# Performance work log

Hardware: AMD Instinct MI355X
Metric: run time of the kernel (lower is better)

The kernel has to match this reference:

```python
import jax, jax.numpy as jnp
import numpy as np

B, T, D = 256, 500, 3   # batch, time steps, input features (time, mag, err)
U, C = 512, 10          # PhasedLSTM units, n_classes
R_ON = 0.05             # open ratio of the phased time gate
ALPHA = 1e-3            # leak rate during closed phase
LN_EPS = 1e-3           # keras LayerNormalization default epsilon


def _glorot(key, shape):
    lim = np.sqrt(6.0 / (shape[0] + shape[1])).astype(np.float32)
    return jax.random.uniform(key, shape, jnp.float32, -lim, lim)


def setup_inputs() -> dict:
    key = jax.random.key(0)
    ks = jax.random.split(key, 12)
    x = jax.random.normal(ks[0], (B, T, D), jnp.float32)
    # monotonically increasing observation times per sample
    times = jnp.cumsum(jax.random.uniform(ks[1], (B, T), jnp.float32), axis=1)
    # layer 0 PhasedLSTM params (gate order i, f, g, o)
    W0 = _glorot(ks[2], (D, 4 * U)); R0 = _glorot(ks[3], (U, 4 * U)); b0 = jnp.zeros((4 * U,), jnp.float32)
    tau0 = jnp.exp(jax.random.uniform(ks[4], (U,), jnp.float32, 0.0, 3.0))
    s0 = jax.random.uniform(ks[5], (U,), jnp.float32) * tau0
    # layer 1
    W1 = _glorot(ks[6], (U, 4 * U)); R1 = _glorot(ks[7], (U, 4 * U)); b1 = jnp.zeros((4 * U,), jnp.float32)
    tau1 = jnp.exp(jax.random.uniform(ks[8], (U,), jnp.float32, 0.0, 3.0))
    s1 = jax.random.uniform(ks[9], (U,), jnp.float32) * tau1
    # per-layer LayerNorm params
    g0 = jnp.ones((U,), jnp.float32); be0 = jnp.zeros((U,), jnp.float32)
    g1 = jnp.ones((U,), jnp.float32); be1 = jnp.zeros((U,), jnp.float32)
    # classifier head
    Wf = _glorot(ks[10], (U, C)); bf = jnp.zeros((C,), jnp.float32)
    return dict(x=x, times=times, W0=W0, R0=R0, b0=b0, tau0=tau0, s0=s0, g0=g0, be0=be0,
                W1=W1, R1=R1, b1=b1, tau1=tau1, s1=s1, g1=g1, be1=be1, Wf=Wf, bf=bf)


def _layernorm(h, g, b):
    m = jnp.mean(h, axis=-1, keepdims=True)
    v = jnp.var(h, axis=-1, keepdims=True)
    return (h - m) * jax.lax.rsqrt(v + LN_EPS) * g + b


def _time_gate(t, tau, s):
    # t: [B], tau/s: [U] -> k: [B, U]
    phi = jnp.mod(t[:, None] - s, tau) / tau
    return jnp.where(phi < 0.5 * R_ON, 2.0 * phi / R_ON,
                     jnp.where(phi < R_ON, 2.0 - 2.0 * phi / R_ON, ALPHA * phi))


def _plstm_step(xi, ti, h, c, W, R, b, tau, s):
    z = xi @ W + h @ R + b                       # [B, 4U]
    i, f, g, o = jnp.split(z, 4, axis=-1)
    i = jax.nn.sigmoid(i); f = jax.nn.sigmoid(f); o = jax.nn.sigmoid(o)
    c_new = f * c + i * jnp.tanh(g)
    h_new = o * jnp.tanh(c_new)
    k = _time_gate(ti, tau, s)                   # phased time gate
    return k * h_new + (1.0 - k) * h, k * c_new + (1.0 - k) * c


def reference(x, times, W0, R0, b0, tau0, s0, g0, be0,
              W1, R1, b1, tau1, s1, g1, be1, Wf, bf):
    xt = jnp.transpose(x, (1, 0, 2))  # [T, B, D]
    tt = times.T                      # [T, B]
    zeros = jnp.zeros((x.shape[0], U), x.dtype)
    init = (zeros, zeros, zeros, zeros)

    def step(carry, inp):
        h0, c0, h1, c1 = carry
        xi, ti = inp
        h0n, c0n = _plstm_step(xi, ti, h0, c0, W0, R0, b0, tau0, s0)
        a0 = _layernorm(h0n, g0, be0)   # normed output feeds next layer; raw state is carried
        h1n, c1n = _plstm_step(a0, ti, h1, c1, W1, R1, b1, tau1, s1)
        a1 = _layernorm(h1n, g1, be1)
        probs = jax.nn.softmax(a1 @ Wf + bf)  # dropout is identity at inference
        return (h0n, c0n, h1n, c1n), probs

    _, out = jax.lax.scan(step, init, (xt, tt))  # out: [T, B, C]
    return jnp.transpose(out, (1, 0, 2))
```

## Files before the change

kernel.cpp:

```cpp
#include <hip/hip_runtime.h>
#include <hip/hip_bf16.h>


#define NB 256
#define NTHR 384
#define T_STEPS 500
#define RON 0.05f
#define ALPHA_LEAK 1e-3f

typedef short short8 __attribute__((ext_vector_type(8)));
typedef float f32x4 __attribute__((ext_vector_type(4)));
typedef unsigned long long ull;

#define OFF_WSWZ 0u
#define OFF_U1   6291456u
#define OFF_V1   6299648u
#define OFF_WFP  6307840u
#define OFF_UFV  6328320u
#define OFF_H0B  6328448u
#define OFF_H1B  6852736u
#define OFF_ST0  7377024u
#define OFF_ST1  7508096u
#define OFF_FLG0 7639168u
#define OFF_FLG1 7640192u
#define ZERO_BYTES 1312768u

#define SMEM_BYTES 156160

#define AT_LD(p)    __hip_atomic_load((p), __ATOMIC_RELAXED, __HIP_MEMORY_SCOPE_AGENT)
#define AT_ST(p, v) __hip_atomic_store((p), (v), __ATOMIC_RELAXED, __HIP_MEMORY_SCOPE_AGENT)

#define G2L(gp, lp) \
  __builtin_amdgcn_global_load_lds( \
      (const __attribute__((address_space(1))) void*)(gp), \
      (__attribute__((address_space(3))) void*)(lp), 16, 0, 16)

__device__ __forceinline__ short f2bf(float x) {
  unsigned u = __float_as_uint(x);
  unsigned r = (u + 0x7fffu + ((u >> 16) & 1u)) >> 16;
  return (short)r;
}
__device__ __forceinline__ float bf2f(short s) {
  return __uint_as_float(((unsigned)(unsigned short)s) << 16);
}
__device__ __forceinline__ float sigm(float x) { return 1.f / (1.f + __expf(-x)); }
__device__ __forceinline__ float tanh_f(float x) {
  float cx = fminf(fmaxf(x, -15.f), 15.f);
  float e = __expf(2.f * cx);
  return (e - 1.f) / (e + 1.f);
}
__device__ __forceinline__ float timegate(float t, float tau, float s) {
  float phi = fmodf(t - s, tau);
  if (phi < 0.f) phi += tau;
  phi /= tau;
  return phi < 0.5f * RON ? (2.f / RON) * phi
       : (phi < RON ? 2.f - (2.f / RON) * phi : ALPHA_LEAK * phi);
}
__device__ __forceinline__ int fragidx(int m, int k) {
  return ((((k >> 5) * 2 + (m >> 4)) * 64) + (((k >> 3) & 3) * 16) + (m & 15)) * 8 + (k & 7);
}

__global__ void prep_weights(const float* __restrict__ R0, const float* __restrict__ W1,
                             const float* __restrict__ R1, const float* __restrict__ g0,
                             short* __restrict__ Wswz) {
  int t = blockIdx.x * 256 + threadIdx.x;
  int lane = t & 63; int rest = t >> 6;
  int nf = rest & 1;  rest >>= 1;
  int kb = rest & 15; rest >>= 4;
  int ch = rest & 1;  rest >>= 1;
  int mm = rest % 3;  int slice = rest / 3;
  int c = ch * 32 + nf * 16 + (lane & 15);
  int gate = c >> 4;
  int unit = slice * 16 + (c & 15);
  int gcol = gate * 512 + unit;
  int k0 = kb * 32 + (lane >> 4) * 8;
  const float* src = (mm == 0) ? R0 : (mm == 1 ? W1 : R1);
  short8 o;
  #pragma unroll
  for (int e = 0; e < 8; ++e) {
    float v = src[(size_t)(k0 + e) * 2048 + gcol];
    if (mm == 1) v *= g0[k0 + e];
    o[e] = f2bf(v);
  }
  *(short8*)(Wswz + (size_t)t * 8) = o;
}

__global__ void prep_vecs(const float* __restrict__ W1, const float* __restrict__ g0,
                          const float* __restrict__ be0,
                          float* __restrict__ u1, float* __restrict__ v1) {
  int c = blockIdx.x * 256 + threadIdx.x;
  float su = 0.f, sv = 0.f;
  for (int k = 0; k < 512; ++k) {
    float w = W1[(size_t)k * 2048 + c];
    su += be0[k] * w; sv += g0[k] * w;
  }
  u1[c] = su; v1[c] = sv;
}

__global__ void prep_head(const float* __restrict__ Wf, const float* __restrict__ g1,
                          const float* __restrict__ be1, const float* __restrict__ bfv,
                          float* __restrict__ Wfp, float* __restrict__ ufv) {
  int t = blockIdx.x * 256 + threadIdx.x;
  if (t < 5120) {
    int kk = t / 640, rem = t - kk * 640, c = rem >> 6, l = rem & 63;
    int k = 8 * l + kk;
    Wfp[t] = g1[k] * Wf[k * 10 + c];
  }
  if (t < 10) {
    float su = bfv[t], sv = 0.f;
    for (int k = 0; k < 512; ++k) {
      float w = Wf[k * 10 + t];
      su += be1[k] * w; sv += g1[k] * w;
    }
    ufv[t] = su; ufv[16 + t] = sv;
  }
}

struct Ptrs {
  const float *x, *times, *W0, *b0, *tau0, *s0, *b1, *tau1, *s1;
  const float *u1v, *v1v, *Wfp, *ufv;
  short *H0b, *H1b;
  float *St0, *St1;
  unsigned *flag0, *flag1;
  float *out;
};

__launch_bounds__(NTHR, 1)
__global__ void plstm_persist(Ptrs P, const short* __restrict__ Wswz) {
  extern __shared__ char smem[];
  short* h0b  = (short*)smem;
  short* h1bL = (short*)(smem + 32768);
  float* h0f  = (float*)(smem + 98304);
  float* c0f = h0f + 512;
  float* h1f = h0f + 1024;
  float* c1f = h0f + 1536;
  float* mu0 = (float*)(smem + 106496); float* rs0 = mu0 + 32;
  float* mu1 = mu0 + 64;                float* rs1 = mu0 + 96;
  float* zbv = (float*)(smem + 107008);
  float* prm = (float*)(smem + 132736);
  float* wfl = (float*)(smem + 134784);
  float* ufl = (float*)(smem + 155264);
  float* xtb = (float*)(smem + 155392);
  float* xtb1 = (float*)(smem + 155904);

  const int tid = threadIdx.x;
  const int g = blockIdx.x & 7;
  const int slice = blockIdx.x >> 3;
  const int wid = tid >> 6, lane = tid & 63;
  const int mm = wid >> 1, ch = wid & 1;
  const int gm0 = g * 32;

  for (int i = tid; i < 2048; i += NTHR) h0f[i] = 0.f;
  for (int i = tid; i < 512; i += NTHR) {
    float v;
    if (i < 192)      { int f = i >> 6, c = i & 63; v = P.W0[f * 2048 + ((c >> 4) << 9) + slice * 16 + (c & 15)]; }
    else if (i < 256) { int c = i & 63; v = P.b0[((c >> 4) << 9) + slice * 16 + (c & 15)]; }
    else if (i < 320) { int c = i & 63; int gc = ((c >> 4) << 9) + slice * 16 + (c & 15);
                        v = P.b1[gc] + P.u1v[gc]; }
    else if (i < 384) { int c = i & 63; v = P.v1v[((c >> 4) << 9) + slice * 16 + (c & 15)]; }
    else if (i < 448) v = 0.f;
    else if (i < 464) v = P.tau0[slice * 16 + (i & 15)];
    else if (i < 480) v = P.s0[slice * 16 + (i & 15)];
    else if (i < 496) v = P.tau1[slice * 16 + (i & 15)];
    else              v = P.s1[slice * 16 + (i & 15)];
    prm[i] = v;
  }
  for (int i = tid; i < 5120; i += NTHR) wfl[i] = P.Wfp[i];
  if (tid < 32) ufl[tid] = P.ufv[tid];

  short8 wr[16][2];
  {
    const short* wb = Wswz + ((((size_t)slice * 3 + mm) * 2 + ch) * 32 * 64) * 8;
    #pragma unroll
    for (int kb = 0; kb < 16; ++kb)
      #pragma unroll
      for (int nf = 0; nf < 2; ++nf) {
        wr[kb][nf] = *(const short8*)(wb + ((kb * 2 + nf) * 64 + lane) * 8);
        asm volatile("" : "+v"(wr[kb][nf]));
      }
  }
  __syncthreads();

  for (int r = 0; r < T_STEPS + 2; ++r) {
    const int bufA = (r + 1) & 1;
    const int bufB = r & 1;
    short* h1s = h1bL + bufB * 16384;

    if (wid == 0) {
      const unsigned tgt = (unsigned)r;
      const unsigned* fp = P.flag0 + g * 32 + (lane & 31);
      for (int it_ = 0; it_ < 100000; ++it_) {
        unsigned v = (lane < 32) ? AT_LD(fp) : 0xFFFFFFFFu;
        if (__all((int)(v >= tgt))) break;
        __builtin_amdgcn_s_sleep(1);
      }
    } else if (wid == 4) {
      int m = lane & 31;
      if (lane < 32) {
        int step = (r < T_STEPS) ? r : (T_STEPS - 1);
        const float* xp = P.x + ((size_t)(gm0 + m) * T_STEPS + step) * 3;
        xtb[m * 4 + 0] = xp[0];
        xtb[m * 4 + 1] = xp[1];
        xtb[m * 4 + 2] = xp[2];
        xtb[m * 4 + 3] = P.times[(size_t)(gm0 + m) * T_STEPS + step];
      } else {
        int s1_ = (r >= 1) ? (r - 1) : 0;
        xtb1[m] = P.times[(size_t)(gm0 + m) * T_STEPS + s1_];
      }
    }
    __syncthreads();

    if (tid < 256) {
      const char* gA = (const char*)(P.H0b + ((size_t)bufA * 8 + g) * 16384);
      const char* gB = (const char*)(P.H1b + ((size_t)bufB * 8 + g) * 16384);
      char* lA = (char*)h0b;
      char* lB = (char*)h1s;
      #pragma unroll
      for (int k = 0; k < 8; ++k) {
        size_t off = (size_t)(k * 256 + tid) * 16;
        G2L(gA + off, lA + off);
        G2L(gB + off, lB + off);
      }
    } else if (wid == 5) {
      const int layer = lane >> 5, m = lane & 31;
      const float* base = layer ? (P.St1 + ((size_t)bufB * 8 + g) * 2048 + m * 64)
                                : (P.St0 + ((size_t)bufA * 8 + g) * 2048 + m * 64);
      const ull* bu = (const ull*)base;
      float s_ = 0.f, q_ = 0.f;
      #pragma unroll
      for (int sl = 0; sl < 32; ++sl) {
        ull v = AT_LD(bu + sl);
        s_ += __uint_as_float((unsigned)v);
        q_ += __uint_as_float((unsigned)(v >> 32));
      }
      float mu = s_ * (1.f / 512.f);
      float var = q_ * (1.f / 512.f) - mu * mu;
      float rs = rsqrtf(var + 1e-3f);
      if (layer == 0) { mu0[m] = mu; rs0[m] = rs; }
      else            { mu1[m] = mu; rs1[m] = rs; }
    }
    __syncthreads();
    float m1r = 0.f, r1r = 0.f;
    if (wid == 1) { m1r = mu1[slice]; r1r = rs1[slice]; }

    {
      f32x4 acc[2][2] = {};
      const short* asrc = (mm == 2) ? h1s : h0b;
      #pragma unroll
      for (int kb = 0; kb < 16; ++kb) {
        short8 a0 = *(const short8*)(asrc + ((kb * 2 + 0) * 64 + lane) * 8);
        short8 a1 = *(const short8*)(asrc + ((kb * 2 + 1) * 64 + lane) * 8);
        #pragma unroll
        for (int nf = 0; nf < 2; ++nf) {
          acc[0][nf] = __builtin_amdgcn_mfma_f32_16x16x32_bf16(a0, wr[kb][nf], acc[0][nf], 0, 0, 0);
          acc[1][nf] = __builtin_amdgcn_mfma_f32_16x16x32_bf16(a1, wr[kb][nf], acc[1][nf], 0, 0, 0);
        }
      }
      float* z = zbv + mm * 2144;
      #pragma unroll
      for (int mf = 0; mf < 2; ++mf)
        #pragma unroll
        for (int nf = 0; nf < 2; ++nf)
          #pragma unroll
          for (int q = 0; q < 4; ++q) {
            int row = mf * 16 + (lane >> 4) * 4 + q;
            int col = ch * 32 + nf * 16 + (lane & 15);
            z[row * 67 + col] = acc[mf][nf][q];
          }
    }
    __syncthreads();

    const bool l0act = (r < T_STEPS);
    const bool l1act = (r >= 1 && r <= T_STEPS);
    if (tid < 256 && l0act) {
      int m = tid >> 3, u0 = (tid & 7) << 1;
      float x0 = xtb[m * 4 + 0], x1 = xtb[m * 4 + 1], x2 = xtb[m * 4 + 2];
      float tmv = xtb[m * 4 + 3];
      unsigned pack = 0;
      float hnv[2];
      #pragma unroll
      for (int uu = 0; uu < 2; ++uu) {
        int u = u0 + uu, id = m * 16 + u;
        float zg4[4];
        #pragma unroll
        for (int q = 0; q < 4; ++q) {
          int c = q * 16 + u;
          zg4[q] = zbv[m * 67 + c] + prm[192 + c]
                 + x0 * prm[c] + x1 * prm[64 + c] + x2 * prm[128 + c];
        }
        float iv = sigm(zg4[0]), fv = sigm(zg4[1]), gv = tanh_f(zg4[2]), ov = sigm(zg4[3]);
        float cold = c0f[id], hold = h0f[id];
        float cp = fv * cold + iv * gv;
        float hp = ov * tanh_f(cp);
        float k = timegate(tmv, prm[448 + u], prm[464 + u]);
        float hn = k * hp + (1.f - k) * hold;
        float cn = k * cp + (1.f - k) * cold;
        h0f[id] = hn; c0f[id] = cn; hnv[uu] = hn;
        pack |= ((unsigned)(unsigned short)f2bf(hn)) << (16 * uu);
      }
      AT_ST((unsigned*)(P.H0b + ((size_t)bufB * 8 + g) * 16384 + fragidx(m, slice * 16 + u0)), pack);
      float sr = hnv[0] + hnv[1], qr = hnv[0] * hnv[0] + hnv[1] * hnv[1];
      sr += __shfl_down(sr, 4, 8); qr += __shfl_down(qr, 4, 8);
      sr += __shfl_down(sr, 2, 8); qr += __shfl_down(qr, 2, 8);
      sr += __shfl_down(sr, 1, 8); qr += __shfl_down(qr, 1, 8);
      if ((tid & 7) == 0) {
        ull pv = ((ull)__float_as_uint(qr) << 32) | __float_as_uint(sr);
        AT_ST((ull*)(P.St0 + ((size_t)bufB * 8 + g) * 2048) + m * 32 + slice, pv);
      }
    }
    #pragma unroll
    for (int pass = 0; pass < 2; ++pass) {
      int idx = -1;
      if (pass == 0 && tid >= 256) idx = tid - 256;
      if (pass == 1 && tid < 128)  idx = 128 + tid;
      if (idx >= 0 && l1act) {
        int m = idx >> 3, u0 = (idx & 7) << 1;
        float mu0m = mu0[m], rs0m = rs0[m];
        float tmv = xtb1[m];
        unsigned pack = 0;
        float hnv[2];
        #pragma unroll
        for (int uu = 0; uu < 2; ++uu) {
          int u = u0 + uu, id = m * 16 + u;
          float zg4[4];
          #pragma unroll
          for (int q = 0; q < 4; ++q) {
            int c = q * 16 + u;
            float zA = zbv[2144 + m * 67 + c];
            float zB = zbv[4288 + m * 67 + c];
            zg4[q] = rs0m * zA + zB + prm[256 + c] - mu0m * rs0m * prm[320 + c];
          }
          float iv = sigm(zg4[0]), fv = sigm(zg4[1]), gv = tanh_f(zg4[2]), ov = sigm(zg4[3]);
          float cold = c1f[id], hold = h1f[id];
          float cp = fv * cold + iv * gv;
          float hp = ov * tanh_f(cp);
          float k = timegate(tmv, prm[480 + u], prm[496 + u]);
          float hn = k * hp + (1.f - k) * hold;
          float cn = k * cp + (1.f - k) * cold;
          h1f[id] = hn; c1f[id] = cn; hnv[uu] = hn;
          pack |= ((unsigned)(unsigned short)f2bf(hn)) << (16 * uu);
        }
        AT_ST((unsigned*)(P.H1b + ((size_t)bufA * 8 + g) * 16384 + fragidx(m, slice * 16 + u0)), pack);
        float sr = hnv[0] + hnv[1], qr = hnv[0] * hnv[0] + hnv[1] * hnv[1];
        sr += __shfl_down(sr, 4, 8); qr += __shfl_down(qr, 4, 8);
        sr += __shfl_down(sr, 2, 8); qr += __shfl_down(qr, 2, 8);
        sr += __shfl_down(sr, 1, 8); qr += __shfl_down(qr, 1, 8);
        if ((idx & 7) == 0) {
          ull pv = ((ull)__float_as_uint(qr) << 32) | __float_as_uint(sr);
          AT_ST((ull*)(P.St1 + ((size_t)bufA * 8 + g) * 2048) + m * 32 + slice, pv);
        }
      }
    }
    __syncthreads();

    if (tid == 0 && r <= T_STEPS) {
      AT_ST(P.flag0 + g * 32 + slice, (unsigned)(r + 1));
    }
    if (wid == 1 && r >= 2) {
      int msam = slice;
      short8 hv8 = *(const short8*)(h1s + fragidx(msam, lane * 8));
      float lg[10];
      #pragma unroll
      for (int c = 0; c < 10; ++c) lg[c] = 0.f;
      #pragma unroll
      for (int kk = 0; kk < 8; ++kk) {
        float hv = bf2f(hv8[kk]);
        const float* wf = wfl + kk * 640 + lane;
        #pragma unroll
        for (int c = 0; c < 10; ++c) lg[c] += hv * wf[c * 64];
      }
      #pragma unroll
      for (int off = 32; off > 0; off >>= 1)
        #pragma unroll
        for (int c = 0; c < 10; ++c) lg[c] += __shfl_down(lg[c], off, 64);
      if (lane == 0) {
        float logit[10], mx = -1e30f;
        #pragma unroll
        for (int c = 0; c < 10; ++c) {
          logit[c] = r1r * lg[c] + ufl[c] - m1r * r1r * ufl[16 + c];
          mx = fmaxf(mx, logit[c]);
        }
        float ssum = 0.f;
        #pragma unroll
        for (int c = 0; c < 10; ++c) { logit[c] = expf(logit[c] - mx); ssum += logit[c]; }
        float inv = 1.f / ssum;
        float* op = P.out + ((size_t)(gm0 + msam) * T_STEPS + (r - 2)) * 10;
        #pragma unroll
        for (int c = 0; c < 10; ++c) op[c] = logit[c] * inv;
      }
    }
  }
}

extern "C" void kernel_launch(void* const* d_in, const int* in_sizes, int n_in,
                              void* d_out, int out_size, void* d_ws, size_t ws_size,
                              hipStream_t stream) {
  const float* x    = (const float*)d_in[0];
  const float* tms  = (const float*)d_in[1];
  const float* W0   = (const float*)d_in[2];
  const float* R0   = (const float*)d_in[3];
  const float* b0   = (const float*)d_in[4];
  const float* tau0 = (const float*)d_in[5];
  const float* s0   = (const float*)d_in[6];
  const float* g0   = (const float*)d_in[7];
  const float* be0  = (const float*)d_in[8];
  const float* W1   = (const float*)d_in[9];
  const float* R1   = (const float*)d_in[10];
  const float* b1   = (const float*)d_in[11];
  const float* tau1 = (const float*)d_in[12];
  const float* s1   = (const float*)d_in[13];
  const float* g1   = (const float*)d_in[14];
  const float* be1  = (const float*)d_in[15];
  const float* Wf   = (const float*)d_in[16];
  const float* bfv  = (const float*)d_in[17];

  char* ws = (char*)d_ws;
  short* Wswz = (short*)(ws + OFF_WSWZ);
  float* u1m  = (float*)(ws + OFF_U1);
  float* v1m  = (float*)(ws + OFF_V1);
  float* Wfpm = (float*)(ws + OFF_WFP);
  float* ufvm = (float*)(ws + OFF_UFV);

  Ptrs P;
  P.x = x; P.times = tms; P.W0 = W0; P.b0 = b0; P.tau0 = tau0; P.s0 = s0;
  P.b1 = b1; P.tau1 = tau1; P.s1 = s1;
  P.u1v = u1m; P.v1v = v1m; P.Wfp = Wfpm; P.ufv = ufvm;
  P.H0b = (short*)(ws + OFF_H0B);
  P.H1b = (short*)(ws + OFF_H1B);
  P.St0 = (float*)(ws + OFF_ST0);
  P.St1 = (float*)(ws + OFF_ST1);
  P.flag0 = (unsigned*)(ws + OFF_FLG0);
  P.flag1 = (unsigned*)(ws + OFF_FLG1);
  P.out = (float*)d_out;

  hipFuncSetAttribute(reinterpret_cast<const void*>(plstm_persist),
                      hipFuncAttributeMaxDynamicSharedMemorySize, SMEM_BYTES);

  prep_weights<<<1536, 256, 0, stream>>>(R0, W1, R1, g0, Wswz);
  prep_vecs<<<8, 256, 0, stream>>>(W1, g0, be0, u1m, v1m);
  prep_head<<<20, 256, 0, stream>>>(Wf, g1, be1, bfv, Wfpm, ufvm);
  hipMemsetAsync(ws + OFF_H0B, 0, ZERO_BYTES, stream);
  plstm_persist<<<NB, NTHR, SMEM_BYTES, stream>>>(P, Wswz);
}
```

Before: 5.245 ms.

## Split each block into two 16-sample half-groups and overlap sync/loads with MFMA

Each persistent block now handles two independent 16-sample sub-groups and alternates between them. While six warps run the recurrent MFMAs and gate math for one sub-group, two extra warps wait on that sub-group's flags, prefetch its hidden state into LDS, and compute LayerNorm statistics for the other. The goal is to hide the cross-block flag wait and global-to-LDS latency behind compute instead of serialising them every step. In exchange the block uses more threads, more double-buffered LDS, and a more involved per-half phase schedule, and each MFMA now uses only a single 16-row fragment.

```diff
diff --git a/kernel.cpp b/kernel.cpp
--- a/kernel.cpp
+++ b/kernel.cpp
@@ -3,7 +3,7 @@
 
 
 #define NB 256
-#define NTHR 384
+#define NTHR 512
 #define T_STEPS 500
 #define RON 0.05f
 #define ALPHA_LEAK 1e-3f
@@ -21,11 +21,10 @@
 #define OFF_H1B  6852736u
 #define OFF_ST0  7377024u
 #define OFF_ST1  7508096u
-#define OFF_FLG0 7639168u
-#define OFF_FLG1 7640192u
+#define OFF_FLG  7639168u
 #define ZERO_BYTES 1312768u
 
-#define SMEM_BYTES 156160
+#define SMEM_BYTES 143872
 
 #define AT_LD(p)    __hip_atomic_load((p), __ATOMIC_RELAXED, __HIP_MEMORY_SCOPE_AGENT)
 #define AT_ST(p, v) __hip_atomic_store((p), (v), __ATOMIC_RELAXED, __HIP_MEMORY_SCOPE_AGENT)
@@ -56,8 +55,8 @@
   return phi < 0.5f * RON ? (2.f / RON) * phi
        : (phi < RON ? 2.f - (2.f / RON) * phi : ALPHA_LEAK * phi);
 }
-__device__ __forceinline__ int fragidx(int m, int k) {
-  return ((((k >> 5) * 2 + (m >> 4)) * 64) + (((k >> 3) & 3) * 16) + (m & 15)) * 8 + (k & 7);
+__device__ __forceinline__ int fragidx16(int m, int k) {
+  return ((k >> 5) * 64 + ((k >> 3) & 3) * 16 + m) * 8 + (k & 7);
 }
 
 __global__ void prep_weights(const float* __restrict__ R0, const float* __restrict__ W1,
@@ -121,36 +120,32 @@
   const float *u1v, *v1v, *Wfp, *ufv;
   short *H0b, *H1b;
   float *St0, *St1;
-  unsigned *flag0, *flag1;
+  unsigned *flag;
   float *out;
 };
 
 __launch_bounds__(NTHR, 1)
 __global__ void plstm_persist(Ptrs P, const short* __restrict__ Wswz) {
   extern __shared__ char smem[];
-  short* h0b  = (short*)smem;
-  short* h1bL = (short*)(smem + 32768);
-  float* h0f  = (float*)(smem + 98304);
-  float* c0f = h0f + 512;
-  float* h1f = h0f + 1024;
-  float* c1f = h0f + 1536;
-  float* mu0 = (float*)(smem + 106496); float* rs0 = mu0 + 32;
-  float* mu1 = mu0 + 64;                float* rs1 = mu0 + 96;
-  float* zbv = (float*)(smem + 107008);
-  float* prm = (float*)(smem + 132736);
-  float* wfl = (float*)(smem + 134784);
-  float* ufl = (float*)(smem + 155264);
-  float* xtb = (float*)(smem + 155392);
-  float* xtb1 = (float*)(smem + 155904);
+  short* h0bs[2] = {(short*)smem, (short*)(smem + 16384)};
+  short* h1bs[2] = {(short*)(smem + 32768), (short*)(smem + 65536)};
+  float* zbv    = (float*)(smem + 98304);
+  float* sts[2] = {(float*)(smem + 111360), (float*)(smem + 115456)};
+  float* mus[2] = {(float*)(smem + 119552), (float*)(smem + 119808)};
+  float* prm    = (float*)(smem + 120064);
+  float* wfl    = (float*)(smem + 122112);
+  float* ufl    = (float*)(smem + 142592);
+  float* xts[2] = {(float*)(smem + 142720), (float*)(smem + 143232)};
 
   const int tid = threadIdx.x;
-  const int g = blockIdx.x & 7;
+  const int pair = blockIdx.x & 7;
   const int slice = blockIdx.x >> 3;
   const int wid = tid >> 6, lane = tid & 63;
   const int mm = wid >> 1, ch = wid & 1;
-  const int gm0 = g * 32;
-
-  for (int i = tid; i < 2048; i += NTHR) h0f[i] = 0.f;
+  const int qgrp[2] = {pair * 2, pair * 2 + 1};
+
+  for (int i = tid; i < 1024; i += NTHR) { sts[0][i] = 0.f; }
+  for (int i = tid; i < 1024; i += NTHR) { sts[1][i] = 0.f; }
   for (int i = tid; i < 512; i += NTHR) {
     float v;
     if (i < 192)      { int f = i >> 6, c = i & 63; v = P.W0[f * 2048 + ((c >> 4) << 9) + slice * 16 + (c & 15)]; }
@@ -169,7 +164,7 @@
   if (tid < 32) ufl[tid] = P.ufv[tid];
 
   short8 wr[16][2];
-  {
+  if (wid < 6) {
     const short* wb = Wswz + ((((size_t)slice * 3 + mm) * 2 + ch) * 32 * 64) * 8;
     #pragma unroll
     for (int kb = 0; kb < 16; ++kb)
@@ -181,212 +176,208 @@
   }
   __syncthreads();
 
-  for (int r = 0; r < T_STEPS + 2; ++r) {
-    const int bufA = (r + 1) & 1;
-    const int bufB = r & 1;
-    short* h1s = h1bL + bufB * 16384;
-
-    if (wid == 0) {
-      const unsigned tgt = (unsigned)r;
-      const unsigned* fp = P.flag0 + g * 32 + (lane & 31);
-      for (int it_ = 0; it_ < 100000; ++it_) {
-        unsigned v = (lane < 32) ? AT_LD(fp) : 0xFFFFFFFFu;
-        if (__all((int)(v >= tgt))) break;
-        __builtin_amdgcn_s_sleep(1);
-      }
-    } else if (wid == 4) {
-      int m = lane & 31;
-      if (lane < 32) {
-        int step = (r < T_STEPS) ? r : (T_STEPS - 1);
-        const float* xp = P.x + ((size_t)(gm0 + m) * T_STEPS + step) * 3;
-        xtb[m * 4 + 0] = xp[0];
-        xtb[m * 4 + 1] = xp[1];
-        xtb[m * 4 + 2] = xp[2];
-        xtb[m * 4 + 3] = P.times[(size_t)(gm0 + m) * T_STEPS + step];
-      } else {
-        int s1_ = (r >= 1) ? (r - 1) : 0;
-        xtb1[m] = P.times[(size_t)(gm0 + m) * T_STEPS + s1_];
-      }
-    }
-    __syncthreads();
-
-    if (tid < 256) {
-      const char* gA = (const char*)(P.H0b + ((size_t)bufA * 8 + g) * 16384);
-      const char* gB = (const char*)(P.H1b + ((size_t)bufB * 8 + g) * 16384);
-      char* lA = (char*)h0b;
-      char* lB = (char*)h1s;
-      #pragma unroll
-      for (int k = 0; k < 8; ++k) {
-        size_t off = (size_t)(k * 256 + tid) * 16;
-        G2L(gA + off, lA + off);
-        G2L(gB + off, lB + off);
-      }
-    } else if (wid == 5) {
-      const int layer = lane >> 5, m = lane & 31;
-      const float* base = layer ? (P.St1 + ((size_t)bufB * 8 + g) * 2048 + m * 64)
-                                : (P.St0 + ((size_t)bufA * 8 + g) * 2048 + m * 64);
-      const ull* bu = (const ull*)base;
-      float s_ = 0.f, q_ = 0.f;
-      #pragma unroll
-      for (int sl = 0; sl < 32; ++sl) {
-        ull v = AT_LD(bu + sl);
-        s_ += __uint_as_float((unsigned)v);
-        q_ += __uint_as_float((unsigned)(v >> 32));
-      }
-      float mu = s_ * (1.f / 512.f);
-      float var = q_ * (1.f / 512.f) - mu * mu;
-      float rs = rsqrtf(var + 1e-3f);
-      if (layer == 0) { mu0[m] = mu; rs0[m] = rs; }
-      else            { mu1[m] = mu; rs1[m] = rs; }
-    }
-    __syncthreads();
-    float m1r = 0.f, r1r = 0.f;
-    if (wid == 1) { m1r = mu1[slice]; r1r = rs1[slice]; }
-
-    {
-      f32x4 acc[2][2] = {};
-      const short* asrc = (mm == 2) ? h1s : h0b;
-      #pragma unroll
-      for (int kb = 0; kb < 16; ++kb) {
-        short8 a0 = *(const short8*)(asrc + ((kb * 2 + 0) * 64 + lane) * 8);
-        short8 a1 = *(const short8*)(asrc + ((kb * 2 + 1) * 64 + lane) * 8);
-        #pragma unroll
-        for (int nf = 0; nf < 2; ++nf) {
-          acc[0][nf] = __builtin_amdgcn_mfma_f32_16x16x32_bf16(a0, wr[kb][nf], acc[0][nf], 0, 0, 0);
-          acc[1][nf] = __builtin_amdgcn_mfma_f32_16x16x32_bf16(a1, wr[kb][nf], acc[1][nf], 0, 0, 0);
+  for (int i = 0; i <= T_STEPS + 2; ++i) {
+    #pragma unroll
+    for (int h = 0; h < 2; ++h) {
+      const int X = h, Y = h ^ 1;
+      const int rs_ = i;
+      const int rc_ = (h == 0) ? i - 1 : i;
+      const bool sv  = (rs_ <= T_STEPS + 1);
+      const bool cv  = (rc_ >= 0 && rc_ <= T_STEPS + 1);
+      const bool mfv = (rc_ >= 0 && rc_ <= T_STEPS);
+      const int qX = qgrp[X], qY = qgrp[Y];
+
+      if (wid < 6) {
+        if (mfv) {
+          f32x4 acc[2] = {};
+          const short* asrc = (mm == 2) ? (h1bs[Y] + (rc_ & 1) * 8192) : h0bs[Y];
+          #pragma unroll
+          for (int kb = 0; kb < 16; ++kb) {
+            short8 a = *(const short8*)(asrc + (kb * 64 + lane) * 8);
+            acc[0] = __builtin_amdgcn_mfma_f32_16x16x32_bf16(a, wr[kb][0], acc[0], 0, 0, 0);
+            acc[1] = __builtin_amdgcn_mfma_f32_16x16x32_bf16(a, wr[kb][1], acc[1], 0, 0, 0);
+          }
+          float* z = zbv + mm * 1088;
+          #pragma unroll
+          for (int nf = 0; nf < 2; ++nf)
+            #pragma unroll
+            for (int q = 0; q < 4; ++q)
+              z[((lane >> 4) * 4 + q) * 67 + ch * 32 + nf * 16 + (lane & 15)] = acc[nf][q];
+        }
+      } else if (sv) {
+        {
+          const unsigned tgt = (unsigned)rs_;
+          const unsigned* fp = P.flag + qX * 32 + (lane & 31);
+          for (int it_ = 0; it_ < 100000; ++it_) {
+            unsigned v = (lane < 32) ? AT_LD(fp) : 0xFFFFFFFFu;
+            if (__all((int)(v >= tgt))) break;
+            __builtin_amdgcn_s_sleep(1);
+          }
+        }
+        const int bufAs = (rs_ + 1) & 1, bufBs = rs_ & 1;
+        if (wid == 6) {
+          const char* gA = (const char*)(P.H0b + ((size_t)bufAs * 16 + qX) * 8192);
+          const char* gB = (const char*)(P.H1b + ((size_t)bufBs * 16 + qX) * 8192);
+          char* lA = (char*)h0bs[X];
+          char* lB = (char*)(h1bs[X] + (rs_ & 1) * 8192);
+          #pragma unroll
+          for (int j = 0; j < 16; ++j) {
+            unsigned off = j * 1024u + (unsigned)lane * 16u;
+            G2L(gA + off, lA + off);
+            G2L(gB + off, lB + off);
+          }
+          int m = lane & 15;
+          if (lane < 16) {
+            int step = (rs_ < T_STEPS) ? rs_ : (T_STEPS - 1);
+            const float* xp = P.x + ((size_t)(qX * 16 + m) * T_STEPS + step) * 3;
+            float* xt = xts[X];
+            xt[m * 4 + 0] = xp[0]; xt[m * 4 + 1] = xp[1]; xt[m * 4 + 2] = xp[2];
+            xt[m * 4 + 3] = P.times[(size_t)(qX * 16 + m) * T_STEPS + step];
+          } else if (lane < 32) {
+            int s1_ = (rs_ >= 1) ? rs_ - 1 : 0;
+            if (s1_ > T_STEPS - 1) s1_ = T_STEPS - 1;
+            xts[X][64 + m] = P.times[(size_t)(qX * 16 + m) * T_STEPS + s1_];
+          }
+        } else {
+          const int layer = lane >> 5, m = lane & 31;
+          if (m < 16) {
+            const float* base = layer
+                ? (P.St1 + ((size_t)bufBs * 16 + qX) * 1024 + m * 64)
+                : (P.St0 + ((size_t)bufAs * 16 + qX) * 1024 + m * 64);
+            const ull* bu = (const ull*)base;
+            float s_ = 0.f, q_ = 0.f;
+            #pragma unroll
+            for (int sl = 0; sl < 32; ++sl) {
+              ull v = AT_LD(bu + sl);
+              s_ += __uint_as_float((unsigned)v);
+              q_ += __uint_as_float((unsigned)(v >> 32));
+            }
+            float mu = s_ * (1.f / 512.f);
+            float var = q_ * (1.f / 512.f) - mu * mu;
+            mus[X][layer * 32 + m] = mu;
+            mus[X][layer * 32 + 16 + m] = rsqrtf(var + 1e-3f);
+          }
         }
       }
-      float* z = zbv + mm * 2144;
-      #pragma unroll
-      for (int mf = 0; mf < 2; ++mf)
-        #pragma unroll
-        for (int nf = 0; nf < 2; ++nf)
-          #pragma unroll
-          for (int q = 0; q < 4; ++q) {
-            int row = mf * 16 + (lane >> 4) * 4 + q;
-            int col = ch * 32 + nf * 16 + (lane & 15);
-            z[row * 67 + col] = acc[mf][nf][q];
-          }
-    }
-    __syncthreads();
-
-    const bool l0act = (r < T_STEPS);
-    const bool l1act = (r >= 1 && r <= T_STEPS);
-    if (tid < 256 && l0act) {
-      int m = tid >> 3, u0 = (tid & 7) << 1;
-      float x0 = xtb[m * 4 + 0], x1 = xtb[m * 4 + 1], x2 = xtb[m * 4 + 2];
-      float tmv = xtb[m * 4 + 3];
-      unsigned pack = 0;
-      float hnv[2];
-      #pragma unroll
-      for (int uu = 0; uu < 2; ++uu) {
-        int u = u0 + uu, id = m * 16 + u;
-        float zg4[4];
-        #pragma unroll
-        for (int q = 0; q < 4; ++q) {
-          int c = q * 16 + u;
-          zg4[q] = zbv[m * 67 + c] + prm[192 + c]
-                 + x0 * prm[c] + x1 * prm[64 + c] + x2 * prm[128 + c];
-        }
-        float iv = sigm(zg4[0]), fv = sigm(zg4[1]), gv = tanh_f(zg4[2]), ov = sigm(zg4[3]);
-        float cold = c0f[id], hold = h0f[id];
-        float cp = fv * cold + iv * gv;
-        float hp = ov * tanh_f(cp);
-        float k = timegate(tmv, prm[448 + u], prm[464 + u]);
-        float hn = k * hp + (1.f - k) * hold;
-        float cn = k * cp + (1.f - k) * cold;
-        h0f[id] = hn; c0f[id] = cn; hnv[uu] = hn;
-        pack |= ((unsigned)(unsigned short)f2bf(hn)) << (16 * uu);
-      }
-      AT_ST((unsigned*)(P.H0b + ((size_t)bufB * 8 + g) * 16384 + fragidx(m, slice * 16 + u0)), pack);
-      float sr = hnv[0] + hnv[1], qr = hnv[0] * hnv[0] + hnv[1] * hnv[1];
-      sr += __shfl_down(sr, 4, 8); qr += __shfl_down(qr, 4, 8);
-      sr += __shfl_down(sr, 2, 8); qr += __shfl_down(qr, 2, 8);
-      sr += __shfl_down(sr, 1, 8); qr += __shfl_down(qr, 1, 8);
-      if ((tid & 7) == 0) {
-        ull pv = ((ull)__float_as_uint(qr) << 32) | __float_as_uint(sr);
-        AT_ST((ull*)(P.St0 + ((size_t)bufB * 8 + g) * 2048) + m * 32 + slice, pv);
-      }
-    }
-    #pragma unroll
-    for (int pass = 0; pass < 2; ++pass) {
-      int idx = -1;
-      if (pass == 0 && tid >= 256) idx = tid - 256;
-      if (pass == 1 && tid < 128)  idx = 128 + tid;
-      if (idx >= 0 && l1act) {
-        int m = idx >> 3, u0 = (idx & 7) << 1;
-        float mu0m = mu0[m], rs0m = rs0[m];
-        float tmv = xtb1[m];
-        unsigned pack = 0;
-        float hnv[2];
-        #pragma unroll
-        for (int uu = 0; uu < 2; ++uu) {
-          int u = u0 + uu, id = m * 16 + u;
-          float zg4[4];
-          #pragma unroll
-          for (int q = 0; q < 4; ++q) {
-            int c = q * 16 + u;
-            float zA = zbv[2144 + m * 67 + c];
-            float zB = zbv[4288 + m * 67 + c];
-            zg4[q] = rs0m * zA + zB + prm[256 + c] - mu0m * rs0m * prm[320 + c];
-          }
-          float iv = sigm(zg4[0]), fv = sigm(zg4[1]), gv = tanh_f(zg4[2]), ov = sigm(zg4[3]);
-          float cold = c1f[id], hold = h1f[id];
-          float cp = fv * cold + iv * gv;
-          float hp = ov * tanh_f(cp);
-          float k = timegate(tmv, prm[480 + u], prm[496 + u]);
-          float hn = k * hp + (1.f - k) * hold;
-          float cn = k * cp + (1.f - k) * cold;
-          h1f[id] = hn; c1f[id] = cn; hnv[uu] = hn;
-          pack |= ((unsigned)(unsigned short)f2bf(hn)) << (16 * uu);
-        }
-        AT_ST((unsigned*)(P.H1b + ((size_t)bufA * 8 + g) * 16384 + fragidx(m, slice * 16 + u0)), pack);
-        float sr = hnv[0] + hnv[1], qr = hnv[0] * hnv[0] + hnv[1] * hnv[1];
-        sr += __shfl_down(sr, 4, 8); qr += __shfl_down(qr, 4, 8);
-        sr += __shfl_down(sr, 2, 8); qr += __shfl_down(qr, 2, 8);
-        sr += __shfl_down(sr, 1, 8); qr += __shfl_down(qr, 1, 8);
-        if ((idx & 7) == 0) {
-          ull pv = ((ull)__float_as_uint(qr) << 32) | __float_as_uint(sr);
-          AT_ST((ull*)(P.St1 + ((size_t)bufA * 8 + g) * 2048) + m * 32 + slice, pv);
+      __syncthreads();
+
+      if (mfv && tid < 256) {
+        const int bufAc = (rc_ + 1) & 1, bufBc = rc_ & 1;
+        const int layer = tid >> 7;
+        const int idx = tid & 127;
+        const int m = idx >> 3, u0 = (idx & 7) << 1;
+        const bool act = (layer == 0) ? (rc_ < T_STEPS) : (rc_ >= 1);
+        if (act) {
+          float* st = sts[Y];
+          float hnv[2]; unsigned pack = 0;
+          if (layer == 0) {
+            const float* xt = xts[Y];
+            float x0 = xt[m * 4], x1 = xt[m * 4 + 1], x2 = xt[m * 4 + 2], tmv = xt[m * 4 + 3];
+            #pragma unroll
+            for (int uu = 0; uu < 2; ++uu) {
+              int u = u0 + uu, id = m * 16 + u;
+              float zg[4];
+              #pragma unroll
+              for (int q = 0; q < 4; ++q) {
+                int c = q * 16 + u;
+                zg[q] = zbv[m * 67 + c] + prm[192 + c]
+                      + x0 * prm[c] + x1 * prm[64 + c] + x2 * prm[128 + c];
+              }
+              float iv = sigm(zg[0]), fv = sigm(zg[1]), gv = tanh_f(zg[2]), ov = sigm(zg[3]);
+              float cold = st[256 + id], hold = st[id];
+              float cp = fv * cold + iv * gv;
+              float hp = ov * tanh_f(cp);
+              float k = timegate(tmv, prm[448 + u], prm[464 + u]);
+              float hn = k * hp + (1.f - k) * hold;
+              float cn = k * cp + (1.f - k) * cold;
+              st[id] = hn; st[256 + id] = cn; hnv[uu] = hn;
+              pack |= ((unsigned)(unsigned short)f2bf(hn)) << (16 * uu);
+            }
+            AT_ST((unsigned*)(P.H0b + ((size_t)bufBc * 16 + qY) * 8192 + fragidx16(m, slice * 16 + u0)), pack);
+            float sr = hnv[0] + hnv[1], qr = hnv[0] * hnv[0] + hnv[1] * hnv[1];
+            sr += __shfl_down(sr, 4, 8); qr += __shfl_down(qr, 4, 8);
+            sr += __shfl_down(sr, 2, 8); qr += __shfl_down(qr, 2, 8);
+            sr += __shfl_down(sr, 1, 8); qr += __shfl_down(qr, 1, 8);
+            if ((idx & 7) == 0) {
+              ull pv = ((ull)__float_as_uint(qr) << 32) | __float_as_uint(sr);
+              AT_ST((ull*)(P.St0 + ((size_t)bufBc * 16 + qY) * 1024) + m * 32 + slice, pv);
+            }
+          } else {
+            float mu0m = mus[Y][m], rs0m = mus[Y][16 + m];
+            float tmv = xts[Y][64 + m];
+            #pragma unroll
+            for (int uu = 0; uu < 2; ++uu) {
+              int u = u0 + uu, id = m * 16 + u;
+              float zg[4];
+              #pragma unroll
+              for (int q = 0; q < 4; ++q) {
+                int c = q * 16 + u;
+                float zA = zbv[1088 + m * 67 + c];
+                float zB = zbv[2176 + m * 67 + c];
+                zg[q] = rs0m * zA + zB + prm[256 + c] - mu0m * rs0m * prm[320 + c];
+              }
+              float iv = sigm(zg[0]), fv = sigm(zg[1]), gv = tanh_f(zg[2]), ov = sigm(zg[3]);
+              float cold = st[768 + id], hold = st[512 + id];
+              float cp = fv * cold + iv * gv;
+              float hp = ov * tanh_f(cp);
+              float k = timegate(tmv, prm[480 + u], prm[496 + u]);
+              float hn = k * hp + (1.f - k) * hold;
+              float cn = k * cp + (1.f - k) * cold;
+              st[512 + id] = hn; st[768 + id] = cn; hnv[uu] = hn;
+              pack |= ((unsigned)(unsigned short)f2bf(hn)) << (16 * uu);
+            }
+            AT_ST((unsigned*)(P.H1b + ((size_t)bufAc * 16 + qY) * 8192 + fragidx16(m, slice * 16 + u0)), pack);
+            float sr = hnv[0] + hnv[1], qr = hnv[0] * hnv[0] + hnv[1] * hnv[1];
+            sr += __shfl_down(sr, 4, 8); qr += __shfl_down(qr, 4, 8);
+            sr += __shfl_down(sr, 2, 8); qr += __shfl_down(qr, 2, 8);
+            sr += __shfl_down(sr, 1, 8); qr += __shfl_down(qr, 1, 8);
+            if ((idx & 7) == 0) {
+              ull pv = ((ull)__float_as_uint(qr) << 32) | __float_as_uint(sr);
+              AT_ST((ull*)(P.St1 + ((size_t)bufAc * 16 + qY) * 1024) + m * 32 + slice, pv);
+            }
+          }
         }
       }
-    }
-    __syncthreads();
-
-    if (tid == 0 && r <= T_STEPS) {
-      AT_ST(P.flag0 + g * 32 + slice, (unsigned)(r + 1));
-    }
-    if (wid == 1 && r >= 2) {
-      int msam = slice;
-      short8 hv8 = *(const short8*)(h1s + fragidx(msam, lane * 8));
-      float lg[10];
-      #pragma unroll
-      for (int c = 0; c < 10; ++c) lg[c] = 0.f;
-      #pragma unroll
-      for (int kk = 0; kk < 8; ++kk) {
-        float hv = bf2f(hv8[kk]);
-        const float* wf = wfl + kk * 640 + lane;
-        #pragma unroll
-        for (int c = 0; c < 10; ++c) lg[c] += hv * wf[c * 64];
-      }
-      #pragma unroll
-      for (int off = 32; off > 0; off >>= 1)
-        #pragma unroll
-        for (int c = 0; c < 10; ++c) lg[c] += __shfl_down(lg[c], off, 64);
-      if (lane == 0) {
-        float logit[10], mx = -1e30f;
-        #pragma unroll
-        for (int c = 0; c < 10; ++c) {
-          logit[c] = r1r * lg[c] + ufl[c] - m1r * r1r * ufl[16 + c];
-          mx = fmaxf(mx, logit[c]);
+      __syncthreads();
+
+      if (cv) {
+        if (tid == 0 && rc_ <= T_STEPS)
+          AT_ST(P.flag + qY * 32 + slice, (unsigned)(rc_ + 1));
+        if (wid == 7 && rc_ >= 2) {
+          const int msam = slice & 15;
+          const short* h1r = h1bs[Y] + (rc_ & 1) * 8192;
+          short8 hv8 = *(const short8*)(h1r + fragidx16(msam, lane * 8));
+          float lg[10];
+          #pragma unroll
+          for (int c = 0; c < 10; ++c) lg[c] = 0.f;
+          #pragma unroll
+          for (int kk = 0; kk < 8; ++kk) {
+            float hv = bf2f(hv8[kk]);
+            const float* wf = wfl + kk * 640 + lane;
+            #pragma unroll
+            for (int c = 0; c < 10; ++c) lg[c] += hv * wf[c * 64];
+          }
+          #pragma unroll
+          for (int off = 32; off > 0; off >>= 1)
+            #pragma unroll
+            for (int c = 0; c < 10; ++c) lg[c] += __shfl_down(lg[c], off, 64);
+          if (lane == 0) {
+            float m1 = mus[Y][32 + msam], r1 = mus[Y][48 + msam];
+            float logit[10], mx = -1e30f;
+            #pragma unroll
+            for (int c = 0; c < 10; ++c) {
+              logit[c] = r1 * lg[c] + ufl[c] - m1 * r1 * ufl[16 + c];
+              mx = fmaxf(mx, logit[c]);
+            }
+            float ssum = 0.f;
+            #pragma unroll
+            for (int c = 0; c < 10; ++c) { logit[c] = expf(logit[c] - mx); ssum += logit[c]; }
+            float inv = 1.f / ssum;
+            float* op = P.out + ((size_t)(qY * 16 + msam) * T_STEPS + (rc_ - 2)) * 10;
+            #pragma unroll
+            for (int c = 0; c < 10; ++c) op[c] = logit[c] * inv;
+          }
         }
-        float ssum = 0.f;
-        #pragma unroll
-        for (int c = 0; c < 10; ++c) { logit[c] = expf(logit[c] - mx); ssum += logit[c]; }
-        float inv = 1.f / ssum;
-        float* op = P.out + ((size_t)(gm0 + msam) * T_STEPS + (r - 2)) * 10;
-        #pragma unroll
-        for (int c = 0; c < 10; ++c) op[c] = logit[c] * inv;
       }
     }
   }
@@ -429,8 +420,7 @@
   P.H1b = (short*)(ws + OFF_H1B);
   P.St0 = (float*)(ws + OFF_ST0);
   P.St1 = (float*)(ws + OFF_ST1);
-  P.flag0 = (unsigned*)(ws + OFF_FLG0);
-  P.flag1 = (unsigned*)(ws + OFF_FLG1);
+  P.flag = (unsigned*)(ws + OFF_FLG);
   P.out = (float*)d_out;
 
   hipFuncSetAttribute(reinterpret_cast<const void*>(plstm_persist),
```

Result: slower. 7.264 ms (+38.5%).
